# Optimization experiments

Measured on AMD Instinct MI355X. Metric: run time of the kernel, lower is better.

## Reference

```python
import jax, jax.numpy as jnp
import numpy as np

C = 1.0
MIN_NORM = 1e-15
BALL_EPS = 4e-3  # hgcn eps for float32 in proj

def _norm(v):
    return jnp.maximum(jnp.linalg.norm(v, axis=-1, keepdims=True), MIN_NORM)

def artanh(y):
    return jnp.arctanh(jnp.clip(y, -1.0 + 1e-7, 1.0 - 1e-7))

def logmap0(p, c):
    sqrt_c = c ** 0.5
    pn = _norm(p)
    return p / (sqrt_c * pn) * artanh(sqrt_c * pn)

def expmap0(u, c):
    sqrt_c = c ** 0.5
    un = _norm(u)
    return jnp.tanh(sqrt_c * un) * u / (sqrt_c * un)

def proj(x, c):
    xn = _norm(x)
    maxnorm = (1.0 - BALL_EPS) / (c ** 0.5)
    return jnp.where(xn > maxnorm, x / xn * maxnorm, x)

def setup_inputs() -> dict:
    key = jax.random.key(0)
    k1, k2, k3, k4 = jax.random.split(key, 4)
    N, E, F = 100000, 640000, 128
    # points inside the Poincare ball
    x = 0.01 * jax.random.normal(k1, (N, F), dtype=jnp.float32)
    adj = jax.random.randint(k2, (2, E), 0, N, dtype=jnp.int64)
    edge_attr = jax.random.normal(k3, (E, F), dtype=jnp.float32)
    att_w = jax.random.normal(k4, (1, 3 * F), dtype=jnp.float32) * (1.0 / np.sqrt(3 * F))
    att_b = jnp.zeros((1,), dtype=jnp.float32)
    return {"x": x, "adj": adj, "edge_attr": edge_attr, "att_w": att_w, "att_b": att_b}

def reference(x, adj, edge_attr, att_w, att_b):
    N = x.shape[0]
    src, dst = adj[0], adj[1]  # agg_direction='in' -> i = 0
    xt = logmap0(x, C)  # [N, F] tangent features
    xs = xt[src]        # [E, F] gathered neighbor tangent feats
    # DenseAtt: sigmoid(Linear(cat(x_i, x_j, edge_attr)))
    feats = jnp.concatenate([xs, xt[dst], edge_attr], axis=-1)  # [E, 3F]
    adj_att = jax.nn.sigmoid(feats @ att_w.T + att_b)           # [E, 1]
    ones = jnp.ones((src.shape[0], 1), dtype=xt.dtype)
    agg_add = jax.ops.segment_sum(xs * adj_att, src, num_segments=N)
    cnt_src = jnp.maximum(jax.ops.segment_sum(ones, src, num_segments=N), 1.0)
    cnt_dst = jnp.maximum(jax.ops.segment_sum(ones, dst, num_segments=N), 1.0)
    mean_src = jax.ops.segment_sum(edge_attr, src, num_segments=N) / cnt_src
    mean_dst = jax.ops.segment_sum(edge_attr, dst, num_segments=N) / cnt_dst
    support_t = xt + agg_add + mean_src + mean_dst
    return proj(expmap0(support_t, C), C)
```

## Files before the change

kernel.cpp:

```cpp
#include <hip/hip_runtime.h>
#include <math.h>

#define F 128
#define WAVE 64
#define CAP 64

__global__ void k_zero(int* __restrict__ p, int n) {
    int i = blockIdx.x * blockDim.x + threadIdx.x;
    if (i < n) p[i] = 0;
}

__device__ __forceinline__ float halfwave_reduce_sum(float v) {
#pragma unroll
    for (int off = 16; off >= 1; off >>= 1)
        v += __shfl_xor(v, off, 64);
    return v;
}

__global__ void k_prenode(const float* __restrict__ x, const float* __restrict__ w,
                          float* __restrict__ a_s, float* __restrict__ a_d, int N) {
    int row = blockIdx.x * (blockDim.x >> 5) + (threadIdx.x >> 5);
    int fl = threadIdx.x & 31;
    if (row >= N) return;
    float4 v = ((const float4*)(x + (size_t)row * F))[fl];
    float ss = halfwave_reduce_sum(v.x * v.x + v.y * v.y + v.z * v.z + v.w * v.w);
    float pn = fmaxf(sqrtf(ss), 1e-15f);
    float y = fminf(pn, 1.0f - 1e-7f);
    float at = 0.5f * logf((1.0f + y) / (1.0f - y));
    float s = at / pn;
    float4 o = make_float4(v.x * s, v.y * s, v.z * s, v.w * s);
    float4 W0 = ((const float4*)w)[fl];
    float4 W1 = ((const float4*)(w + F))[fl];
    float d0 = halfwave_reduce_sum(o.x * W0.x + o.y * W0.y + o.z * W0.z + o.w * W0.w);
    float d1 = halfwave_reduce_sum(o.x * W1.x + o.y * W1.y + o.z * W1.z + o.w * W1.w);
    if (fl == 0) { a_s[row] = d0; a_d[row] = d1; }
}

__global__ void k_fill(const int* __restrict__ src, const int* __restrict__ dst,
                       int* __restrict__ cur_src, int* __restrict__ cur_dst,
                       int* __restrict__ elist_src, int* __restrict__ elist_dst, int E) {
    int e = blockIdx.x * blockDim.x + threadIdx.x;
    if (e >= E) return;
    int s = src[e], d = dst[e];
    int ps = atomicAdd(&cur_src[s], 1);
    if (ps < CAP) elist_src[(size_t)s * CAP + ps] = e;
    int pd = atomicAdd(&cur_dst[d], 1);
    if (pd < CAP) elist_dst[(size_t)d * CAP + pd] = e;
}

__global__ void k_aggfinal(const float* __restrict__ x, const float* __restrict__ eattr,
                           const int* __restrict__ dst,
                           const int* __restrict__ cur_src, const int* __restrict__ cur_dst,
                           const int* __restrict__ elist_src, const int* __restrict__ elist_dst,
                           const float* __restrict__ a_s, const float* __restrict__ a_d,
                           const float* __restrict__ w, const float* __restrict__ bptr,
                           float* __restrict__ out, int N) {
    int n = blockIdx.x * (blockDim.x / WAVE) + (threadIdx.x / WAVE);
    int lane = threadIdx.x & (WAVE - 1);
    if (n >= N) return;
    int half = lane >> 5;
    int fl   = lane & 31;

    int cS = cur_src[n]; int degS = cS < CAP ? cS : CAP;
    int cD = cur_dst[n]; int degD = cD < CAP ? cD : CAP;
    int e_lnS = (lane < degS) ? elist_src[(size_t)n * CAP + lane] : 0;
    int e_lnD = (lane < degD) ? elist_dst[(size_t)n * CAP + lane] : 0;
    int dstv  = (lane < degS) ? dst[e_lnS] : 0;
    float advl = (lane < degS) ? a_d[dstv] : 0.f;

    float4 W2 = ((const float4*)(w + 2 * F))[fl];
    float a_sn = a_s[n];
    float bias = bptr[0];

    float4 accS = make_float4(0.f, 0.f, 0.f, 0.f);
    float4 accD = make_float4(0.f, 0.f, 0.f, 0.f);
    float attsum = 0.f;
    int degM = degS > degD ? degS : degD;
    for (int i = 0; i < degM; i += 2) {
        int idx = i + half;
        int eS = __shfl(e_lnS, idx, 64);
        int eD = __shfl(e_lnD, idx, 64);
        float adv = __shfl(advl, idx, 64);
        if (idx < degD) {
            float4 v = ((const float4*)(eattr + (size_t)eD * F))[fl];
            accD.x += v.x; accD.y += v.y; accD.z += v.z; accD.w += v.w;
        }
        if (idx < degS) {
            float4 v = ((const float4*)(eattr + (size_t)eS * F))[fl];
            accS.x += v.x; accS.y += v.y; accS.z += v.z; accS.w += v.w;
            float p = halfwave_reduce_sum(v.x * W2.x + v.y * W2.y + v.z * W2.z + v.w * W2.w);
            float tot = a_sn + adv + p + bias;
            attsum += 1.0f / (1.0f + expf(-tot));
        }
    }
    accS.x += __shfl_xor(accS.x, 32, 64); accS.y += __shfl_xor(accS.y, 32, 64);
    accS.z += __shfl_xor(accS.z, 32, 64); accS.w += __shfl_xor(accS.w, 32, 64);
    accD.x += __shfl_xor(accD.x, 32, 64); accD.y += __shfl_xor(accD.y, 32, 64);
    accD.z += __shfl_xor(accD.z, 32, 64); accD.w += __shfl_xor(accD.w, 32, 64);
    attsum += __shfl_xor(attsum, 32, 64);

    float4 xv = ((const float4*)(x + (size_t)n * F))[fl];
    float ssx = halfwave_reduce_sum(xv.x * xv.x + xv.y * xv.y + xv.z * xv.z + xv.w * xv.w);
    float pnx = fmaxf(sqrtf(ssx), 1e-15f);
    float yx = fminf(pnx, 1.0f - 1e-7f);
    float atx = 0.5f * logf((1.0f + yx) / (1.0f - yx));
    float sx = atx / pnx;

    float invS = 1.0f / fmaxf((float)cS, 1.0f);
    float invD = 1.0f / fmaxf((float)cD, 1.0f);
    float fa = (1.0f + attsum) * sx;
    float4 u;
    u.x = xv.x * fa + accS.x * invS + accD.x * invD;
    u.y = xv.y * fa + accS.y * invS + accD.y * invD;
    u.z = xv.z * fa + accS.z * invS + accD.z * invD;
    u.w = xv.w * fa + accS.w * invS + accD.w * invD;

    float pp = halfwave_reduce_sum(u.x * u.x + u.y * u.y + u.z * u.z + u.w * u.w);
    float un = fmaxf(sqrtf(pp), 1e-15f);
    float t = tanhf(un);
    float scale = fminf(t, 1.0f - 4e-3f) / un;
    if (half == 0) {
        float4 o = make_float4(u.x * scale, u.y * scale, u.z * scale, u.w * scale);
        ((float4*)(out + (size_t)n * F))[fl] = o;
    }
}

extern "C" void kernel_launch(void* const* d_in, const int* in_sizes, int n_in,
                              void* d_out, int out_size, void* d_ws, size_t ws_size,
                              hipStream_t stream) {
    const float* x      = (const float*)d_in[0];
    const int*   adj    = (const int*)d_in[1];
    const float* eattr  = (const float*)d_in[2];
    const float* att_w  = (const float*)d_in[3];
    const float* att_b  = (const float*)d_in[4];
    float* out = (float*)d_out;

    const int N = in_sizes[0] / F;
    const int E = in_sizes[1] / 2;
    const int* src = adj;
    const int* dst = adj + E;

    char* ws = (char*)d_ws;
    size_t off = 0;
    float* a_s       = (float*)(ws + off); off += (size_t)N * sizeof(float);
    float* a_d       = (float*)(ws + off); off += (size_t)N * sizeof(float);
    int*   elist_src = (int*)  (ws + off); off += (size_t)N * CAP * sizeof(int);
    int*   elist_dst = (int*)  (ws + off); off += (size_t)N * CAP * sizeof(int);
    int*   zblock    = (int*)  (ws + off);
    int*   cur_src   = zblock;
    int*   cur_dst   = zblock + N;

    dim3 blk(256);
    const int RPB = 256 / WAVE;
    const int HPB = 256 / 32;

    k_zero    <<<(2 * N + 255) / 256, blk, 0, stream>>>(zblock, 2 * N);
    k_prenode <<<(N + HPB - 1) / HPB, blk, 0, stream>>>(x, att_w, a_s, a_d, N);
    k_fill    <<<(E + 255) / 256, blk, 0, stream>>>(src, dst, cur_src, cur_dst,
                                                    elist_src, elist_dst, E);
    k_aggfinal<<<(N + RPB - 1) / RPB, blk, 0, stream>>>(x, eattr, dst,
                cur_src, cur_dst, elist_src, elist_dst, a_s, a_d, att_w, att_b, out, N);
}
```

Baseline: 274.6 us.

## Precompute per-edge attention and gather fp16 edge features in aggregation

Adds a pre-pass that streams edge_attr once, computes each edge's dot product with the attention weights, and writes an fp16 copy of the edge features. The fill kernel then computes the per-edge sigmoid attention, and the aggregation kernel gathers half-precision rows and sums precomputed attention instead of doing per-edge reductions. The zero, node-prep and edge-prep kernels merge into a single launch, and fast-math exp/log plus an exp-based tanh replace the library calls. This trades an extra full write and read of edge features for smaller random gathers, and loses precision in the edge sums.

```diff
diff --git a/kernel.cpp b/kernel.cpp
--- a/kernel.cpp
+++ b/kernel.cpp
@@ -1,14 +1,10 @@
 #include <hip/hip_runtime.h>
+#include <hip/hip_fp16.h>
 #include <math.h>
 
 #define F 128
 #define WAVE 64
 #define CAP 64
-
-__global__ void k_zero(int* __restrict__ p, int n) {
-    int i = blockIdx.x * blockDim.x + threadIdx.x;
-    if (i < n) p[i] = 0;
-}
 
 __device__ __forceinline__ float halfwave_reduce_sum(float v) {
 #pragma unroll
@@ -17,45 +13,74 @@
     return v;
 }
 
-__global__ void k_prenode(const float* __restrict__ x, const float* __restrict__ w,
-                          float* __restrict__ a_s, float* __restrict__ a_d, int N) {
-    int row = blockIdx.x * (blockDim.x >> 5) + (threadIdx.x >> 5);
-    int fl = threadIdx.x & 31;
-    if (row >= N) return;
-    float4 v = ((const float4*)(x + (size_t)row * F))[fl];
-    float ss = halfwave_reduce_sum(v.x * v.x + v.y * v.y + v.z * v.z + v.w * v.w);
-    float pn = fmaxf(sqrtf(ss), 1e-15f);
-    float y = fminf(pn, 1.0f - 1e-7f);
-    float at = 0.5f * logf((1.0f + y) / (1.0f - y));
-    float s = at / pn;
-    float4 o = make_float4(v.x * s, v.y * s, v.z * s, v.w * s);
-    float4 W0 = ((const float4*)w)[fl];
-    float4 W1 = ((const float4*)(w + F))[fl];
-    float d0 = halfwave_reduce_sum(o.x * W0.x + o.y * W0.y + o.z * W0.z + o.w * W0.w);
-    float d1 = halfwave_reduce_sum(o.x * W1.x + o.y * W1.y + o.z * W1.z + o.w * W1.w);
-    if (fl == 0) { a_s[row] = d0; a_d[row] = d1; }
+__global__ void k_pre(const float* __restrict__ x, const float* __restrict__ eattr,
+                      const float* __restrict__ w,
+                      ushort* __restrict__ eah, float* __restrict__ dea,
+                      float* __restrict__ a_s, float* __restrict__ a_d,
+                      int* __restrict__ zptr,
+                      int B1, int B2, int N, int E) {
+    int b = blockIdx.x;
+    if (b < B1) {
+        int r = b * 8 + (threadIdx.x >> 5);
+        int fl = threadIdx.x & 31;
+        if (r >= E) return;
+        float4 v = ((const float4*)(eattr + (size_t)r * F))[fl];
+        float4 W = ((const float4*)(w + 2 * F))[fl];
+        float p = halfwave_reduce_sum(v.x * W.x + v.y * W.y + v.z * W.z + v.w * W.w);
+        if (fl == 0) dea[r] = p;
+        __half2 h01 = __float22half2_rn(make_float2(v.x, v.y));
+        __half2 h23 = __float22half2_rn(make_float2(v.z, v.w));
+        uint2 pk;
+        pk.x = *(unsigned int*)&h01;
+        pk.y = *(unsigned int*)&h23;
+        ((uint2*)(eah + (size_t)r * F))[fl] = pk;
+    } else if (b < B1 + B2) {
+        int row = (b - B1) * 8 + (threadIdx.x >> 5);
+        int fl = threadIdx.x & 31;
+        if (row >= N) return;
+        float4 v = ((const float4*)(x + (size_t)row * F))[fl];
+        float ss = halfwave_reduce_sum(v.x * v.x + v.y * v.y + v.z * v.z + v.w * v.w);
+        float pn = fmaxf(sqrtf(ss), 1e-15f);
+        float y = fminf(pn, 1.0f - 1e-7f);
+        float at = 0.5f * __logf((1.0f + y) / (1.0f - y));
+        float s = at / pn;
+        float4 o = make_float4(v.x * s, v.y * s, v.z * s, v.w * s);
+        float4 W0 = ((const float4*)w)[fl];
+        float4 W1 = ((const float4*)(w + F))[fl];
+        float d0 = halfwave_reduce_sum(o.x * W0.x + o.y * W0.y + o.z * W0.z + o.w * W0.w);
+        float d1 = halfwave_reduce_sum(o.x * W1.x + o.y * W1.y + o.z * W1.z + o.w * W1.w);
+        if (fl == 0) { a_s[row] = d0; a_d[row] = d1; }
+    } else {
+        int i = (b - B1 - B2) * 256 + threadIdx.x;
+        if (i < 2 * N) zptr[i] = 0;
+    }
 }
 
 __global__ void k_fill(const int* __restrict__ src, const int* __restrict__ dst,
+                       const float* __restrict__ dea,
+                       const float* __restrict__ a_s, const float* __restrict__ a_d,
+                       const float* __restrict__ bptr,
                        int* __restrict__ cur_src, int* __restrict__ cur_dst,
-                       int* __restrict__ elist_src, int* __restrict__ elist_dst, int E) {
+                       int* __restrict__ elist_src, int* __restrict__ elist_dst,
+                       float* __restrict__ att_e, int E) {
     int e = blockIdx.x * blockDim.x + threadIdx.x;
     if (e >= E) return;
     int s = src[e], d = dst[e];
+    float tot = a_s[s] + a_d[d] + dea[e] + bptr[0];
+    att_e[e] = 1.0f / (1.0f + __expf(-tot));
     int ps = atomicAdd(&cur_src[s], 1);
     if (ps < CAP) elist_src[(size_t)s * CAP + ps] = e;
     int pd = atomicAdd(&cur_dst[d], 1);
     if (pd < CAP) elist_dst[(size_t)d * CAP + pd] = e;
 }
 
-__global__ void k_aggfinal(const float* __restrict__ x, const float* __restrict__ eattr,
-                           const int* __restrict__ dst,
-                           const int* __restrict__ cur_src, const int* __restrict__ cur_dst,
-                           const int* __restrict__ elist_src, const int* __restrict__ elist_dst,
-                           const float* __restrict__ a_s, const float* __restrict__ a_d,
-                           const float* __restrict__ w, const float* __restrict__ bptr,
-                           float* __restrict__ out, int N) {
-    int n = blockIdx.x * (blockDim.x / WAVE) + (threadIdx.x / WAVE);
+__global__ __launch_bounds__(256) void
+k_aggfinal(const float* __restrict__ x, const ushort* __restrict__ eah,
+           const int* __restrict__ cur_src, const int* __restrict__ cur_dst,
+           const int* __restrict__ elist_src, const int* __restrict__ elist_dst,
+           const float* __restrict__ att_e,
+           float* __restrict__ out, int N) {
+    int n = blockIdx.x * 4 + (threadIdx.x >> 6);
     int lane = threadIdx.x & (WAVE - 1);
     if (n >= N) return;
     int half = lane >> 5;
@@ -65,45 +90,42 @@
     int cD = cur_dst[n]; int degD = cD < CAP ? cD : CAP;
     int e_lnS = (lane < degS) ? elist_src[(size_t)n * CAP + lane] : 0;
     int e_lnD = (lane < degD) ? elist_dst[(size_t)n * CAP + lane] : 0;
-    int dstv  = (lane < degS) ? dst[e_lnS] : 0;
-    float advl = (lane < degS) ? a_d[dstv] : 0.f;
-
-    float4 W2 = ((const float4*)(w + 2 * F))[fl];
-    float a_sn = a_s[n];
-    float bias = bptr[0];
+    float attl = (lane < degS) ? att_e[e_lnS] : 0.f;
+    float attsum = attl;
+#pragma unroll
+    for (int off = 32; off >= 1; off >>= 1)
+        attsum += __shfl_xor(attsum, off, 64);
 
     float4 accS = make_float4(0.f, 0.f, 0.f, 0.f);
     float4 accD = make_float4(0.f, 0.f, 0.f, 0.f);
-    float attsum = 0.f;
     int degM = degS > degD ? degS : degD;
     for (int i = 0; i < degM; i += 2) {
         int idx = i + half;
         int eS = __shfl(e_lnS, idx, 64);
         int eD = __shfl(e_lnD, idx, 64);
-        float adv = __shfl(advl, idx, 64);
         if (idx < degD) {
-            float4 v = ((const float4*)(eattr + (size_t)eD * F))[fl];
-            accD.x += v.x; accD.y += v.y; accD.z += v.z; accD.w += v.w;
+            uint2 pk = ((const uint2*)(eah + (size_t)eD * F))[fl];
+            float2 f01 = __half22float2(*(__half2*)&pk.x);
+            float2 f23 = __half22float2(*(__half2*)&pk.y);
+            accD.x += f01.x; accD.y += f01.y; accD.z += f23.x; accD.w += f23.y;
         }
         if (idx < degS) {
-            float4 v = ((const float4*)(eattr + (size_t)eS * F))[fl];
-            accS.x += v.x; accS.y += v.y; accS.z += v.z; accS.w += v.w;
-            float p = halfwave_reduce_sum(v.x * W2.x + v.y * W2.y + v.z * W2.z + v.w * W2.w);
-            float tot = a_sn + adv + p + bias;
-            attsum += 1.0f / (1.0f + expf(-tot));
+            uint2 pk = ((const uint2*)(eah + (size_t)eS * F))[fl];
+            float2 f01 = __half22float2(*(__half2*)&pk.x);
+            float2 f23 = __half22float2(*(__half2*)&pk.y);
+            accS.x += f01.x; accS.y += f01.y; accS.z += f23.x; accS.w += f23.y;
         }
     }
     accS.x += __shfl_xor(accS.x, 32, 64); accS.y += __shfl_xor(accS.y, 32, 64);
     accS.z += __shfl_xor(accS.z, 32, 64); accS.w += __shfl_xor(accS.w, 32, 64);
     accD.x += __shfl_xor(accD.x, 32, 64); accD.y += __shfl_xor(accD.y, 32, 64);
     accD.z += __shfl_xor(accD.z, 32, 64); accD.w += __shfl_xor(accD.w, 32, 64);
-    attsum += __shfl_xor(attsum, 32, 64);
 
     float4 xv = ((const float4*)(x + (size_t)n * F))[fl];
     float ssx = halfwave_reduce_sum(xv.x * xv.x + xv.y * xv.y + xv.z * xv.z + xv.w * xv.w);
     float pnx = fmaxf(sqrtf(ssx), 1e-15f);
     float yx = fminf(pnx, 1.0f - 1e-7f);
-    float atx = 0.5f * logf((1.0f + yx) / (1.0f - yx));
+    float atx = 0.5f * __logf((1.0f + yx) / (1.0f - yx));
     float sx = atx / pnx;
 
     float invS = 1.0f / fmaxf((float)cS, 1.0f);
@@ -117,7 +139,8 @@
 
     float pp = halfwave_reduce_sum(u.x * u.x + u.y * u.y + u.z * u.z + u.w * u.w);
     float un = fmaxf(sqrtf(pp), 1e-15f);
-    float t = tanhf(un);
+    float ex = __expf(2.0f * un);
+    float t = 1.0f - 2.0f / (ex + 1.0f);
     float scale = fminf(t, 1.0f - 4e-3f) / un;
     if (half == 0) {
         float4 o = make_float4(u.x * scale, u.y * scale, u.z * scale, u.w * scale);
@@ -142,22 +165,26 @@
 
     char* ws = (char*)d_ws;
     size_t off = 0;
-    float* a_s       = (float*)(ws + off); off += (size_t)N * sizeof(float);
-    float* a_d       = (float*)(ws + off); off += (size_t)N * sizeof(float);
-    int*   elist_src = (int*)  (ws + off); off += (size_t)N * CAP * sizeof(int);
-    int*   elist_dst = (int*)  (ws + off); off += (size_t)N * CAP * sizeof(int);
-    int*   zblock    = (int*)  (ws + off);
+    ushort* eah      = (ushort*)(ws + off); off += (size_t)E * F * sizeof(ushort);
+    int*   elist_src = (int*)   (ws + off); off += (size_t)N * CAP * sizeof(int);
+    int*   elist_dst = (int*)   (ws + off); off += (size_t)N * CAP * sizeof(int);
+    float* a_s       = (float*) (ws + off); off += (size_t)N * sizeof(float);
+    float* a_d       = (float*) (ws + off); off += (size_t)N * sizeof(float);
+    float* dea       = (float*) (ws + off); off += (size_t)E * sizeof(float);
+    float* att_e     = (float*) (ws + off); off += (size_t)E * sizeof(float);
+    int*   zblock    = (int*)   (ws + off);
     int*   cur_src   = zblock;
     int*   cur_dst   = zblock + N;
 
     dim3 blk(256);
-    const int RPB = 256 / WAVE;
-    const int HPB = 256 / 32;
+    const int B1 = (E + 7) / 8;
+    const int B2 = (N + 7) / 8;
+    const int B3 = (2 * N + 255) / 256;
 
-    k_zero    <<<(2 * N + 255) / 256, blk, 0, stream>>>(zblock, 2 * N);
-    k_prenode <<<(N + HPB - 1) / HPB, blk, 0, stream>>>(x, att_w, a_s, a_d, N);
-    k_fill    <<<(E + 255) / 256, blk, 0, stream>>>(src, dst, cur_src, cur_dst,
-                                                    elist_src, elist_dst, E);
-    k_aggfinal<<<(N + RPB - 1) / RPB, blk, 0, stream>>>(x, eattr, dst,
-                cur_src, cur_dst, elist_src, elist_dst, a_s, a_d, att_w, att_b, out, N);
+    k_pre     <<<B1 + B2 + B3, blk, 0, stream>>>(x, eattr, att_w, eah, dea,
+                a_s, a_d, zblock, B1, B2, N, E);
+    k_fill    <<<(E + 255) / 256, blk, 0, stream>>>(src, dst, dea, a_s, a_d, att_b,
+                cur_src, cur_dst, elist_src, elist_dst, att_e, E);
+    k_aggfinal<<<(N + 3) / 4, blk, 0, stream>>>(x, eah,
+                cur_src, cur_dst, elist_src, elist_dst, att_e, out, N);
 }
```

Result: slower. 298.3 us (+8.6%).
